# Performance work log

Hardware: AMD Instinct MI355X
Metric: run time of the kernel (lower is better)

Reference implementation:

```python
import jax, jax.numpy as jnp
import numpy as np

N_NODES = 20000
L_MAX = 6
R_IN = 256
R_HID = 512
R_OUT = 256
LEAKY_SLOPE = 0.01  # torch.nn.functional.leaky_relu default


def setup_inputs() -> dict:
    key = jax.random.key(0)
    k1, k2, k3, k4 = jax.random.split(key, 4)
    x = jax.random.normal(k1, (N_NODES, R_IN, L_MAX * 2), dtype=jnp.float32)
    # per-node rotation angles -> per-degree 2x2 rotation matrices (k*theta for degree k)
    theta = jax.random.uniform(k2, (N_NODES,), dtype=jnp.float32, minval=0.0, maxval=2.0 * np.pi)
    ang = theta[:, None] * jnp.arange(1, L_MAX + 1, dtype=jnp.float32)[None, :]  # (n, L)
    c, s = jnp.cos(ang), jnp.sin(ang)
    rot_theta = jnp.stack([jnp.stack([c, -s], axis=-1),
                           jnp.stack([s, c], axis=-1)], axis=-2)  # (n, L, 2, 2)
    # xavier_normal: std = sqrt(2 / (fan_in + fan_out))
    W1 = jax.random.normal(k3, (L_MAX, R_HID, R_IN), dtype=jnp.float32) * np.sqrt(2.0 / (R_IN + R_HID))
    W2 = jax.random.normal(k4, (L_MAX, R_OUT, R_HID), dtype=jnp.float32) * np.sqrt(2.0 / (R_HID + R_OUT))
    return {"x": x, "rot_theta": rot_theta, "W1": W1, "W2": W2}


def so2_linear(x, W, r_out):
    # x: (n, r_in, L_max*2); W: (L_max, r_out, r_in)
    n = x.shape[0]
    x4 = x.reshape(n, -1, L_MAX, 2)              # (n, r_in, L, 2)
    out = jnp.einsum('nilc,loi->nolc', x4, W)    # fused block-diagonal GEMM over degrees
    return out.reshape(n, r_out, L_MAX * 2)


def rot_activation(x, rot):
    # rotate each degree-l 2-vector into local frame, apply leaky_relu, rotate back
    n = x.shape[0]
    x4 = x.reshape(n, -1, L_MAX, 2)                      # (n, r, L, 2)
    a = jnp.einsum('njlm,nlmc->njlc', x4, rot)           # x @ R per (node, degree)
    a = jnp.where(a >= 0, a, LEAKY_SLOPE * a)            # pointwise leaky_relu
    out = jnp.einsum('njlc,nlmc->njlm', a, rot)          # (act) @ R^T  (inverse rotation)
    return out.reshape(x.shape)


def reference(x, rot_theta, W1, W2):
    h = so2_linear(x, W1, R_HID)
    h = rot_activation(h, rot_theta)
    return so2_linear(h, W2, R_OUT)
```

## Files before the change

### kernel.cpp

```cpp
#include <hip/hip_runtime.h>
#include <stdint.h>


#define LMAX 6
#define NN 20000
#define RIN 256
#define RHID 512
#define ROUT 256
#define MTILE 64
#define NMT 626
#define MPAD (NMT*MTILE)

#define A2_STRIDE 272
#define GE_STRIDE 528

typedef __attribute__((ext_vector_type(8))) short short8;
typedef __attribute__((ext_vector_type(4))) float f32x4;

__device__ __forceinline__ uint16_t f2bf(float f) {
  uint32_t x = __builtin_bit_cast(uint32_t, f);
  x += 0x7fffu + ((x >> 16) & 1u);
  return (uint16_t)(x >> 16);
}
__device__ __forceinline__ float bf2f(uint16_t u) {
  return __builtin_bit_cast(float, ((uint32_t)u) << 16);
}

__device__ __forceinline__ f32x4 mfma16(short8 a, short8 b, f32x4 c) {
  return __builtin_amdgcn_mfma_f32_16x16x32_bf16(a, b, c, 0, 0, 0);
}

__global__ void prep_weights(const float* __restrict__ W1, const float* __restrict__ W2,
                             uint16_t* __restrict__ w1f, uint16_t* __restrict__ w2f) {
  int idx = blockIdx.x * 256 + threadIdx.x;
  if (idx >= LMAX * RHID * RIN) return;
  {
    int l = idx / (RHID * RIN);
    int rem = idx - l * (RHID * RIN);
    int o = rem >> 8;
    int i = rem & 255;
    int lane = ((i >> 3) & 3) * 16 + (o & 15);
    size_t dst = (size_t)l * (RHID * RIN) +
                 ((((size_t)(o >> 4) * 8 + (i >> 5)) * 64 + lane) * 8 + (i & 7));
    w1f[dst] = f2bf(W1[idx]);
  }
  {
    int l = idx / (ROUT * RHID);
    int rem = idx - l * (ROUT * RHID);
    int o = rem >> 9;
    int j = rem & 511;
    int lane = ((j >> 3) & 3) * 16 + (o & 15);
    size_t dst = (size_t)l * (ROUT * RHID) +
                 ((((size_t)(o >> 4) * 16 + (j >> 5)) * 64 + lane) * 8 + (j & 7));
    w2f[dst] = f2bf(W2[idx]);
  }
}

__global__ void prep_x(const float* __restrict__ x, const float* __restrict__ rot,
                       uint16_t* __restrict__ xr) {
  int t = blockIdx.x * 256 + threadIdx.x;
  if (t >= NN * RIN) return;
  int n = t >> 8, i = t & 255;
  const float4* xp = (const float4*)(x + (size_t)t * 12);
  float4 v0 = xp[0], v1 = xp[1], v2 = xp[2];
  float xv[12] = {v0.x, v0.y, v0.z, v0.w, v1.x, v1.y, v1.z, v1.w, v2.x, v2.y, v2.z, v2.w};
  const float* rp = rot + (size_t)n * 24;
#pragma unroll
  for (int l = 0; l < LMAX; ++l) {
    float c0 = xv[2 * l], c1 = xv[2 * l + 1];
    float r00 = rp[4 * l + 0], r01 = rp[4 * l + 1];
    float r10 = rp[4 * l + 2], r11 = rp[4 * l + 3];
    float a0 = c0 * r00 + c1 * r10;
    float a1 = c0 * r01 + c1 * r11;
    size_t base = (size_t)l * MPAD * RIN + (size_t)(2 * n) * RIN + i;
    xr[base] = f2bf(a0);
    xr[base + RIN] = f2bf(a1);
  }
}

__global__ __launch_bounds__(512, 4) void so2_gemm(
    const uint16_t* __restrict__ xr,
    const uint16_t* __restrict__ w1f,
    const uint16_t* __restrict__ w2f,
    uint16_t* __restrict__ g) {
  __shared__ alignas(16) uint8_t SH[32768 + MTILE * A2_STRIDE];
  uint8_t* XsB = SH;
  uint8_t* A2B = SH + 32768;

  const int l = blockIdx.y;
  const int m0 = blockIdx.x * MTILE;
  const int tid = threadIdx.x;
  const int lane = tid & 63;
  const int wid = tid >> 6;
  const int l15 = lane & 15;
  const int l4 = lane >> 4;

  const char* xsrc = (const char*)(xr + (size_t)l * MPAD * RIN + (size_t)m0 * RIN);
#pragma unroll
  for (int it = 0; it < 4; ++it) {
    int off = it * 8192 + tid * 16;
    int row = off >> 9;
    int colb = off & 511;
    short8 v = *(const short8*)(xsrc + off);
    *(short8*)(XsB + row * 512 + (colb ^ ((row & 7) << 4))) = v;
  }
  __syncthreads();

  const uint16_t* w1p = w1f + (size_t)l * RHID * RIN;
  const uint16_t* w2p = w2f + (size_t)l * ROUT * RHID;

  f32x4 acc2[4][2];
#pragma unroll
  for (int a = 0; a < 4; ++a)
#pragma unroll
    for (int b = 0; b < 2; ++b)
      acc2[a][b] = (f32x4){0.f, 0.f, 0.f, 0.f};

#pragma unroll 1
  for (int oc = 0; oc < 4; ++oc) {
    f32x4 acc1[4];
#pragma unroll
    for (int a = 0; a < 4; ++a) acc1[a] = (f32x4){0.f, 0.f, 0.f, 0.f};

    const uint16_t* w1c = w1p + (((size_t)(oc * 8 + wid) * 8) * 64) * 8;
#pragma unroll
    for (int ks = 0; ks < 8; ++ks) {
      short8 bfr = *(const short8*)(w1c + ((size_t)ks * 64 + lane) * 8);
#pragma unroll
      for (int mf = 0; mf < 4; ++mf) {
        int row = mf * 16 + l15;
        int colb = ks * 64 + l4 * 16;
        short8 af = *(const short8*)(XsB + row * 512 + (colb ^ ((row & 7) << 4)));
        acc1[mf] = mfma16(af, bfr, acc1[mf]);
      }
    }

    __syncthreads();
#pragma unroll
    for (int mf = 0; mf < 4; ++mf)
#pragma unroll
      for (int r = 0; r < 4; ++r) {
        int row = mf * 16 + l4 * 4 + r;
        float v = acc1[mf][r];
        v = v >= 0.f ? v : 0.01f * v;
        *(uint16_t*)(A2B + row * A2_STRIDE + (wid * 16 + l15) * 2) = f2bf(v);
      }
    __syncthreads();

#pragma unroll
    for (int ks2 = 0; ks2 < 4; ++ks2) {
      short8 a2[4];
#pragma unroll
      for (int mf = 0; mf < 4; ++mf)
        a2[mf] = *(const short8*)(A2B + (mf * 16 + l15) * A2_STRIDE + ks2 * 64 + l4 * 16);
      short8 b2[2];
#pragma unroll
      for (int fc2 = 0; fc2 < 2; ++fc2) {
        int ofrag2 = wid * 2 + fc2;
        int kstep = oc * 4 + ks2;
        b2[fc2] = *(const short8*)(w2p + (((size_t)(ofrag2 * 16 + kstep)) * 64 + lane) * 8);
      }
#pragma unroll
      for (int mf = 0; mf < 4; ++mf)
#pragma unroll
        for (int fc2 = 0; fc2 < 2; ++fc2)
          acc2[mf][fc2] = mfma16(a2[mf], b2[fc2], acc2[mf][fc2]);
    }
  }

  __syncthreads();
#pragma unroll
  for (int mf = 0; mf < 4; ++mf)
#pragma unroll
    for (int fc2 = 0; fc2 < 2; ++fc2)
#pragma unroll
      for (int r = 0; r < 4; ++r) {
        int row = mf * 16 + l4 * 4 + r;
        int col = wid * 32 + fc2 * 16 + l15;
        *(uint16_t*)(SH + row * GE_STRIDE + col * 2) = f2bf(acc2[mf][fc2][r]);
      }
  __syncthreads();

  char* gdst = (char*)(g + (size_t)l * MPAD * ROUT + (size_t)m0 * ROUT);
#pragma unroll
  for (int it = 0; it < 4; ++it) {
    int off = it * 8192 + tid * 16;
    int row = off >> 9;
    int colb = off & 511;
    short8 v = *(const short8*)(SH + row * GE_STRIDE + colb);
    *(short8*)(gdst + off) = v;
  }
}

__global__ void post_out(const uint16_t* __restrict__ g, const float* __restrict__ rot,
                         float* __restrict__ out) {
  int n = blockIdx.x;
  int o = threadIdx.x;
  const float* rp = rot + (size_t)n * 24;
  float res[12];
#pragma unroll
  for (int l = 0; l < LMAX; ++l) {
    size_t base = (size_t)l * MPAD * ROUT + (size_t)(2 * n) * ROUT + o;
    float g0 = bf2f(g[base]);
    float g1 = bf2f(g[base + ROUT]);
    res[2 * l]     = rp[4 * l + 0] * g0 + rp[4 * l + 1] * g1;
    res[2 * l + 1] = rp[4 * l + 2] * g0 + rp[4 * l + 3] * g1;
  }
  float4* op = (float4*)(out + (size_t)(n * 256 + o) * 12);
  op[0] = make_float4(res[0], res[1], res[2], res[3]);
  op[1] = make_float4(res[4], res[5], res[6], res[7]);
  op[2] = make_float4(res[8], res[9], res[10], res[11]);
}

extern "C" void kernel_launch(void* const* d_in, const int* in_sizes, int n_in,
                              void* d_out, int out_size, void* d_ws, size_t ws_size,
                              hipStream_t stream) {
  (void)in_sizes; (void)n_in; (void)out_size;
  const float* x   = (const float*)d_in[0];
  const float* rot = (const float*)d_in[1];
  const float* W1  = (const float*)d_in[2];
  const float* W2  = (const float*)d_in[3];
  float* out = (float*)d_out;

  const size_t xr_elems = (size_t)LMAX * MPAD * RIN;
  const size_t w_elems  = (size_t)LMAX * RHID * RIN;
  if (ws_size < (size_t)LMAX * MPAD * ROUT * 2) return;

  uint16_t* xr  = (uint16_t*)d_out;
  uint16_t* w1f = xr + xr_elems;
  uint16_t* w2f = w1f + w_elems;
  uint16_t* g   = (uint16_t*)d_ws;

  prep_weights<<<3072, 256, 0, stream>>>(W1, W2, w1f, w2f);
  prep_x<<<20000, 256, 0, stream>>>(x, rot, xr);
  dim3 gg(NMT, LMAX);
  so2_gemm<<<gg, 512, 0, stream>>>(xr, w1f, w2f, g);
  post_out<<<20000, 256, 0, stream>>>(g, rot, out);
}
```

Baseline: 309.6 us.

## Persist GEMM blocks over multiple M tiles with double-buffered hidden activations

Each block of the fused two-GEMM kernel now handles four consecutive 64-row tiles instead of one. The hidden activation buffer is double-buffered so the second GEMM on one chunk overlaps the first GEMM on the next, which halves the barriers per chunk. Waves are rearranged into a 2x4 grid in place of 1x8, and the output is written straight from registers instead of being staged through shared memory. This trades fewer blocks (about 157x6) and more LDS per block for less barrier stalling and more register reuse, but the uncoalesced 2-byte global stores and lower parallelism could hurt.

After: 593.3 us. 91.6% more time.

```diff
diff --git a/kernel.cpp b/kernel.cpp
--- a/kernel.cpp
+++ b/kernel.cpp
@@ -10,9 +10,10 @@
 #define MTILE 64
 #define NMT 626
 #define MPAD (NMT*MTILE)
+#define TILES 4
+#define NBX ((NMT + TILES - 1) / TILES)
 
 #define A2_STRIDE 272
-#define GE_STRIDE 528
 
 typedef __attribute__((ext_vector_type(8))) short short8;
 typedef __attribute__((ext_vector_type(4))) float f32x4;
@@ -83,113 +84,143 @@
     const uint16_t* __restrict__ w1f,
     const uint16_t* __restrict__ w2f,
     uint16_t* __restrict__ g) {
-  __shared__ alignas(16) uint8_t SH[32768 + MTILE * A2_STRIDE];
-  uint8_t* XsB = SH;
-  uint8_t* A2B = SH + 32768;
+  __shared__ alignas(16) uint8_t Xs[MTILE * 512];
+  __shared__ alignas(16) uint8_t A2[2][MTILE * A2_STRIDE];
 
   const int l = blockIdx.y;
-  const int m0 = blockIdx.x * MTILE;
+  const int tile0 = blockIdx.x * TILES;
+  const int Tv = min(TILES, NMT - tile0);
   const int tid = threadIdx.x;
   const int lane = tid & 63;
   const int wid = tid >> 6;
+  const int wn = wid & 3;
+  const int wm = wid >> 2;
   const int l15 = lane & 15;
   const int l4 = lane >> 4;
 
-  const char* xsrc = (const char*)(xr + (size_t)l * MPAD * RIN + (size_t)m0 * RIN);
-#pragma unroll
-  for (int it = 0; it < 4; ++it) {
-    int off = it * 8192 + tid * 16;
-    int row = off >> 9;
-    int colb = off & 511;
-    short8 v = *(const short8*)(xsrc + off);
-    *(short8*)(XsB + row * 512 + (colb ^ ((row & 7) << 4))) = v;
-  }
+  const uint16_t* w1p = w1f + (size_t)l * (RHID * RIN);
+  const uint16_t* w2p = w2f + (size_t)l * (ROUT * RHID);
+  const uint16_t* xrl = xr + (size_t)l * MPAD * RIN;
+  uint16_t* gl = g + (size_t)l * MPAD * ROUT;
+
+  f32x4 acc1[2][2];
+  f32x4 acc2[2][4];
+#pragma unroll
+  for (int a = 0; a < 2; ++a)
+#pragma unroll
+    for (int b = 0; b < 4; ++b) acc2[a][b] = (f32x4){0.f, 0.f, 0.f, 0.f};
+
+  auto STAGE = [&](int t) {
+    const char* xsrc = (const char*)(xrl + (size_t)(tile0 + t) * MTILE * RIN);
+#pragma unroll
+    for (int it = 0; it < 4; ++it) {
+      int off = it * 8192 + tid * 16;
+      int row = off >> 9;
+      int colb = off & 511;
+      short8 v = *(const short8*)(xsrc + off);
+      *(short8*)(Xs + row * 512 + (colb ^ ((row & 7) << 4))) = v;
+    }
+  };
+
+  auto G1 = [&](int oc) {
+#pragma unroll
+    for (int a = 0; a < 2; ++a)
+#pragma unroll
+      for (int b = 0; b < 2; ++b) acc1[a][b] = (f32x4){0.f, 0.f, 0.f, 0.f};
+    const uint16_t* w1c0 = w1p + (size_t)(oc * 8 + wn * 2) * (8 * 64 * 8);
+    const uint16_t* w1c1 = w1c0 + 8 * 64 * 8;
+#pragma unroll
+    for (int ks = 0; ks < 8; ++ks) {
+      short8 b0 = *(const short8*)(w1c0 + ((size_t)ks * 64 + lane) * 8);
+      short8 b1 = *(const short8*)(w1c1 + ((size_t)ks * 64 + lane) * 8);
+#pragma unroll
+      for (int mf = 0; mf < 2; ++mf) {
+        int row = wm * 32 + mf * 16 + l15;
+        int colb = ks * 64 + l4 * 16;
+        short8 a = *(const short8*)(Xs + row * 512 + (colb ^ ((row & 7) << 4)));
+        acc1[mf][0] = mfma16(a, b0, acc1[mf][0]);
+        acc1[mf][1] = mfma16(a, b1, acc1[mf][1]);
+      }
+    }
+  };
+
+  auto WA2 = [&](int oc) {
+    uint8_t* buf = A2[oc & 1];
+#pragma unroll
+    for (int mf = 0; mf < 2; ++mf)
+#pragma unroll
+      for (int fc = 0; fc < 2; ++fc)
+#pragma unroll
+        for (int r = 0; r < 4; ++r) {
+          int row = wm * 32 + mf * 16 + l4 * 4 + r;
+          int col = wn * 32 + fc * 16 + l15;
+          float v = acc1[mf][fc][r];
+          v = v >= 0.f ? v : 0.01f * v;
+          *(uint16_t*)(buf + row * A2_STRIDE + col * 2) = f2bf(v);
+        }
+  };
+
+  auto G2 = [&](int oc) {
+    const uint8_t* buf = A2[oc & 1];
+#pragma unroll
+    for (int ks2 = 0; ks2 < 4; ++ks2) {
+      short8 a2[2];
+#pragma unroll
+      for (int mf = 0; mf < 2; ++mf)
+        a2[mf] = *(const short8*)(buf + (wm * 32 + mf * 16 + l15) * A2_STRIDE +
+                                  ks2 * 64 + l4 * 16);
+#pragma unroll
+      for (int nf = 0; nf < 4; ++nf) {
+        short8 b = *(const short8*)(w2p + ((size_t)((wn * 4 + nf) * 16 + oc * 4 + ks2) * 64 + lane) * 8);
+#pragma unroll
+        for (int mf = 0; mf < 2; ++mf)
+          acc2[mf][nf] = mfma16(a2[mf], b, acc2[mf][nf]);
+      }
+    }
+  };
+
+  auto EPI = [&](int t) {
+    uint16_t* gb = gl + (size_t)(tile0 + t) * MTILE * ROUT;
+#pragma unroll
+    for (int mf = 0; mf < 2; ++mf)
+#pragma unroll
+      for (int nf = 0; nf < 4; ++nf) {
+#pragma unroll
+        for (int r = 0; r < 4; ++r) {
+          int row = wm * 32 + mf * 16 + l4 * 4 + r;
+          int col = wn * 64 + nf * 16 + l15;
+          gb[(size_t)row * ROUT + col] = f2bf(acc2[mf][nf][r]);
+        }
+        acc2[mf][nf] = (f32x4){0.f, 0.f, 0.f, 0.f};
+      }
+  };
+
+  STAGE(0);
   __syncthreads();
-
-  const uint16_t* w1p = w1f + (size_t)l * RHID * RIN;
-  const uint16_t* w2p = w2f + (size_t)l * ROUT * RHID;
-
-  f32x4 acc2[4][2];
-#pragma unroll
-  for (int a = 0; a < 4; ++a)
-#pragma unroll
-    for (int b = 0; b < 2; ++b)
-      acc2[a][b] = (f32x4){0.f, 0.f, 0.f, 0.f};
-
-#pragma unroll 1
-  for (int oc = 0; oc < 4; ++oc) {
-    f32x4 acc1[4];
-#pragma unroll
-    for (int a = 0; a < 4; ++a) acc1[a] = (f32x4){0.f, 0.f, 0.f, 0.f};
-
-    const uint16_t* w1c = w1p + (((size_t)(oc * 8 + wid) * 8) * 64) * 8;
-#pragma unroll
-    for (int ks = 0; ks < 8; ++ks) {
-      short8 bfr = *(const short8*)(w1c + ((size_t)ks * 64 + lane) * 8);
-#pragma unroll
-      for (int mf = 0; mf < 4; ++mf) {
-        int row = mf * 16 + l15;
-        int colb = ks * 64 + l4 * 16;
-        short8 af = *(const short8*)(XsB + row * 512 + (colb ^ ((row & 7) << 4)));
-        acc1[mf] = mfma16(af, bfr, acc1[mf]);
-      }
-    }
-
-    __syncthreads();
-#pragma unroll
-    for (int mf = 0; mf < 4; ++mf)
-#pragma unroll
-      for (int r = 0; r < 4; ++r) {
-        int row = mf * 16 + l4 * 4 + r;
-        float v = acc1[mf][r];
-        v = v >= 0.f ? v : 0.01f * v;
-        *(uint16_t*)(A2B + row * A2_STRIDE + (wid * 16 + l15) * 2) = f2bf(v);
-      }
-    __syncthreads();
-
-#pragma unroll
-    for (int ks2 = 0; ks2 < 4; ++ks2) {
-      short8 a2[4];
-#pragma unroll
-      for (int mf = 0; mf < 4; ++mf)
-        a2[mf] = *(const short8*)(A2B + (mf * 16 + l15) * A2_STRIDE + ks2 * 64 + l4 * 16);
-      short8 b2[2];
-#pragma unroll
-      for (int fc2 = 0; fc2 < 2; ++fc2) {
-        int ofrag2 = wid * 2 + fc2;
-        int kstep = oc * 4 + ks2;
-        b2[fc2] = *(const short8*)(w2p + (((size_t)(ofrag2 * 16 + kstep)) * 64 + lane) * 8);
-      }
-#pragma unroll
-      for (int mf = 0; mf < 4; ++mf)
-#pragma unroll
-        for (int fc2 = 0; fc2 < 2; ++fc2)
-          acc2[mf][fc2] = mfma16(a2[mf], b2[fc2], acc2[mf][fc2]);
-    }
-  }
-
+  G1(0);
+  WA2(0);
   __syncthreads();
-#pragma unroll
-  for (int mf = 0; mf < 4; ++mf)
-#pragma unroll
-    for (int fc2 = 0; fc2 < 2; ++fc2)
-#pragma unroll
-      for (int r = 0; r < 4; ++r) {
-        int row = mf * 16 + l4 * 4 + r;
-        int col = wid * 32 + fc2 * 16 + l15;
-        *(uint16_t*)(SH + row * GE_STRIDE + col * 2) = f2bf(acc2[mf][fc2][r]);
-      }
-  __syncthreads();
-
-  char* gdst = (char*)(g + (size_t)l * MPAD * ROUT + (size_t)m0 * ROUT);
-#pragma unroll
-  for (int it = 0; it < 4; ++it) {
-    int off = it * 8192 + tid * 16;
-    int row = off >> 9;
-    int colb = off & 511;
-    short8 v = *(const short8*)(SH + row * GE_STRIDE + colb);
-    *(short8*)(gdst + off) = v;
-  }
+
+  for (int c = 1; c < 4 * Tv; ++c) {
+    int oc = c & 3;
+    if (oc == 0) {
+      int t = c >> 2;
+      G2(3);
+      STAGE(t);
+      EPI(t - 1);
+      __syncthreads();
+      G1(0);
+      WA2(0);
+      __syncthreads();
+    } else {
+      G2(oc - 1);
+      G1(oc);
+      WA2(oc);
+      __syncthreads();
+    }
+  }
+  G2(3);
+  EPI(Tv - 1);
 }
 
 __global__ void post_out(const uint16_t* __restrict__ g, const float* __restrict__ rot,
@@ -233,7 +264,7 @@
 
   prep_weights<<<3072, 256, 0, stream>>>(W1, W2, w1f, w2f);
   prep_x<<<20000, 256, 0, stream>>>(x, rot, xr);
-  dim3 gg(NMT, LMAX);
+  dim3 gg(NBX, LMAX);
   so2_gemm<<<gg, 512, 0, stream>>>(xr, w1f, w2f, g);
   post_out<<<20000, 256, 0, stream>>>(g, rot, out);
 }
```

## Switch fused SO2 GEMM to 32x32x16 MFMA with larger hidden chunks and XOR swizzle

Applied to the files above, without the earlier changes.

Replaces the 16x16x32 bf16 MFMA tiles with 32x32x16 tiles, repacking both weight matrices into the matching fragment layout. The hidden dimension is now processed in two chunks of 256 instead of four of 128, and the second GEMM splits waves 2x4 over rows and output columns. A full XOR swizzle replaces the padded LDS strides, and the output staging reuses the input buffer. The aim is fewer LDS fragment reads per FLOP and fewer barriers per tile. In exchange, the kernel holds larger accumulators per wave and uses 64KB of LDS, which may lower occupancy.

New measurement: 541.1 us. +74.7%, slower.

```diff
diff --git a/kernel.cpp b/kernel.cpp
--- a/kernel.cpp
+++ b/kernel.cpp
@@ -11,11 +11,8 @@
 #define NMT 626
 #define MPAD (NMT*MTILE)
 
-#define A2_STRIDE 272
-#define GE_STRIDE 528
-
 typedef __attribute__((ext_vector_type(8))) short short8;
-typedef __attribute__((ext_vector_type(4))) float f32x4;
+typedef __attribute__((ext_vector_type(16))) float f32x16;
 
 __device__ __forceinline__ uint16_t f2bf(float f) {
   uint32_t x = __builtin_bit_cast(uint32_t, f);
@@ -26,8 +23,12 @@
   return __builtin_bit_cast(float, ((uint32_t)u) << 16);
 }
 
-__device__ __forceinline__ f32x4 mfma16(short8 a, short8 b, f32x4 c) {
-  return __builtin_amdgcn_mfma_f32_16x16x32_bf16(a, b, c, 0, 0, 0);
+__device__ __forceinline__ f32x16 mfma32(short8 a, short8 b, f32x16 c) {
+  return __builtin_amdgcn_mfma_f32_32x32x16_bf16(a, b, c, 0, 0, 0);
+}
+
+__device__ __forceinline__ int swz512(int row, int colb) {
+  return row * 512 + ((((colb >> 4) ^ row) & 31) << 4) + (colb & 15);
 }
 
 __global__ void prep_weights(const float* __restrict__ W1, const float* __restrict__ W2,
@@ -39,9 +40,9 @@
     int rem = idx - l * (RHID * RIN);
     int o = rem >> 8;
     int i = rem & 255;
-    int lane = ((i >> 3) & 3) * 16 + (o & 15);
+    int lane = ((i >> 3) & 1) * 32 + (o & 31);
     size_t dst = (size_t)l * (RHID * RIN) +
-                 ((((size_t)(o >> 4) * 8 + (i >> 5)) * 64 + lane) * 8 + (i & 7));
+                 ((((size_t)(o >> 5) * 16 + (i >> 4)) * 64 + lane) * 8 + (i & 7));
     w1f[dst] = f2bf(W1[idx]);
   }
   {
@@ -49,9 +50,9 @@
     int rem = idx - l * (ROUT * RHID);
     int o = rem >> 9;
     int j = rem & 511;
-    int lane = ((j >> 3) & 3) * 16 + (o & 15);
+    int lane = ((j >> 3) & 1) * 32 + (o & 31);
     size_t dst = (size_t)l * (ROUT * RHID) +
-                 ((((size_t)(o >> 4) * 16 + (j >> 5)) * 64 + lane) * 8 + (j & 7));
+                 ((((size_t)(o >> 5) * 32 + (j >> 4)) * 64 + lane) * 8 + (j & 7));
     w2f[dst] = f2bf(W2[idx]);
   }
 }
@@ -83,17 +84,21 @@
     const uint16_t* __restrict__ w1f,
     const uint16_t* __restrict__ w2f,
     uint16_t* __restrict__ g) {
-  __shared__ alignas(16) uint8_t SH[32768 + MTILE * A2_STRIDE];
-  uint8_t* XsB = SH;
-  uint8_t* A2B = SH + 32768;
+  __shared__ alignas(16) uint8_t Xs[MTILE * 512];
+  __shared__ alignas(16) uint8_t A2[MTILE * 512];
 
   const int l = blockIdx.y;
   const int m0 = blockIdx.x * MTILE;
   const int tid = threadIdx.x;
   const int lane = tid & 63;
   const int wid = tid >> 6;
-  const int l15 = lane & 15;
-  const int l4 = lane >> 4;
+  const int l31 = lane & 31;
+  const int lh = lane >> 5;
+  const int wm = wid & 1;
+  const int wn4 = wid >> 1;
+
+  const uint16_t* w1p = w1f + (size_t)l * (RHID * RIN);
+  const uint16_t* w2p = w2f + (size_t)l * (ROUT * RHID);
 
   const char* xsrc = (const char*)(xr + (size_t)l * MPAD * RIN + (size_t)m0 * RIN);
 #pragma unroll
@@ -102,83 +107,76 @@
     int row = off >> 9;
     int colb = off & 511;
     short8 v = *(const short8*)(xsrc + off);
-    *(short8*)(XsB + row * 512 + (colb ^ ((row & 7) << 4))) = v;
-  }
-  __syncthreads();
-
-  const uint16_t* w1p = w1f + (size_t)l * RHID * RIN;
-  const uint16_t* w2p = w2f + (size_t)l * ROUT * RHID;
-
-  f32x4 acc2[4][2];
-#pragma unroll
-  for (int a = 0; a < 4; ++a)
-#pragma unroll
-    for (int b = 0; b < 2; ++b)
-      acc2[a][b] = (f32x4){0.f, 0.f, 0.f, 0.f};
-
-#pragma unroll 1
-  for (int oc = 0; oc < 4; ++oc) {
-    f32x4 acc1[4];
-#pragma unroll
-    for (int a = 0; a < 4; ++a) acc1[a] = (f32x4){0.f, 0.f, 0.f, 0.f};
-
-    const uint16_t* w1c = w1p + (((size_t)(oc * 8 + wid) * 8) * 64) * 8;
-#pragma unroll
-    for (int ks = 0; ks < 8; ++ks) {
-      short8 bfr = *(const short8*)(w1c + ((size_t)ks * 64 + lane) * 8);
-#pragma unroll
-      for (int mf = 0; mf < 4; ++mf) {
-        int row = mf * 16 + l15;
-        int colb = ks * 64 + l4 * 16;
-        short8 af = *(const short8*)(XsB + row * 512 + (colb ^ ((row & 7) << 4)));
-        acc1[mf] = mfma16(af, bfr, acc1[mf]);
+    *(short8*)(Xs + swz512(row, colb)) = v;
+  }
+  __syncthreads();
+
+  f32x16 acc1[2];
+  f32x16 acc2[2];
+#pragma unroll
+  for (int a = 0; a < 2; ++a) acc2[a] = (f32x16)(0.f);
+
+  auto G1 = [&](int oc) {
+#pragma unroll
+    for (int a = 0; a < 2; ++a) acc1[a] = (f32x16)(0.f);
+    const uint16_t* wc = w1p + (size_t)(oc * 8 + wid) * (16 * 64 * 8);
+#pragma unroll
+    for (int ks = 0; ks < 16; ++ks) {
+      short8 b = *(const short8*)(wc + ((size_t)ks * 64 + lane) * 8);
+#pragma unroll
+      for (int mf = 0; mf < 2; ++mf) {
+        int row = mf * 32 + l31;
+        short8 a = *(const short8*)(Xs + swz512(row, ks * 32 + lh * 16));
+        acc1[mf] = mfma32(a, b, acc1[mf]);
       }
     }
-
-    __syncthreads();
-#pragma unroll
-    for (int mf = 0; mf < 4; ++mf)
-#pragma unroll
-      for (int r = 0; r < 4; ++r) {
-        int row = mf * 16 + l4 * 4 + r;
+  };
+
+  auto WA2 = [&]() {
+#pragma unroll
+    for (int mf = 0; mf < 2; ++mf)
+#pragma unroll
+      for (int r = 0; r < 16; ++r) {
+        int row = mf * 32 + (r & 3) + 8 * (r >> 2) + 4 * lh;
+        int colb = (wid * 32 + l31) * 2;
         float v = acc1[mf][r];
         v = v >= 0.f ? v : 0.01f * v;
-        *(uint16_t*)(A2B + row * A2_STRIDE + (wid * 16 + l15) * 2) = f2bf(v);
+        *(uint16_t*)(A2 + swz512(row, colb)) = f2bf(v);
       }
-    __syncthreads();
-
-#pragma unroll
-    for (int ks2 = 0; ks2 < 4; ++ks2) {
-      short8 a2[4];
-#pragma unroll
-      for (int mf = 0; mf < 4; ++mf)
-        a2[mf] = *(const short8*)(A2B + (mf * 16 + l15) * A2_STRIDE + ks2 * 64 + l4 * 16);
-      short8 b2[2];
-#pragma unroll
-      for (int fc2 = 0; fc2 < 2; ++fc2) {
-        int ofrag2 = wid * 2 + fc2;
-        int kstep = oc * 4 + ks2;
-        b2[fc2] = *(const short8*)(w2p + (((size_t)(ofrag2 * 16 + kstep)) * 64 + lane) * 8);
+  };
+
+  auto G2 = [&](int oc) {
+#pragma unroll
+    for (int ks = 0; ks < 16; ++ks) {
+      int row = wm * 32 + l31;
+      short8 a = *(const short8*)(A2 + swz512(row, ks * 32 + lh * 16));
+#pragma unroll
+      for (int nf = 0; nf < 2; ++nf) {
+        short8 b = *(const short8*)(w2p +
+            ((size_t)((wn4 * 2 + nf) * 32 + oc * 16 + ks) * 64 + lane) * 8);
+        acc2[nf] = mfma32(a, b, acc2[nf]);
       }
-#pragma unroll
-      for (int mf = 0; mf < 4; ++mf)
-#pragma unroll
-        for (int fc2 = 0; fc2 < 2; ++fc2)
-          acc2[mf][fc2] = mfma16(a2[mf], b2[fc2], acc2[mf][fc2]);
     }
-  }
-
-  __syncthreads();
-#pragma unroll
-  for (int mf = 0; mf < 4; ++mf)
-#pragma unroll
-    for (int fc2 = 0; fc2 < 2; ++fc2)
-#pragma unroll
-      for (int r = 0; r < 4; ++r) {
-        int row = mf * 16 + l4 * 4 + r;
-        int col = wid * 32 + fc2 * 16 + l15;
-        *(uint16_t*)(SH + row * GE_STRIDE + col * 2) = f2bf(acc2[mf][fc2][r]);
-      }
+  };
+
+  G1(0);
+  WA2();
+  __syncthreads();
+  G2(0);
+  G1(1);
+  __syncthreads();
+  WA2();
+  __syncthreads();
+  G2(1);
+
+#pragma unroll
+  for (int nf = 0; nf < 2; ++nf)
+#pragma unroll
+    for (int r = 0; r < 16; ++r) {
+      int row = wm * 32 + (r & 3) + 8 * (r >> 2) + 4 * lh;
+      int colb = ((wn4 * 2 + nf) * 32 + l31) * 2;
+      *(uint16_t*)(Xs + swz512(row, colb)) = f2bf(acc2[nf][r]);
+    }
   __syncthreads();
 
   char* gdst = (char*)(g + (size_t)l * MPAD * ROUT + (size_t)m0 * ROUT);
@@ -187,7 +185,7 @@
     int off = it * 8192 + tid * 16;
     int row = off >> 9;
     int colb = off & 511;
-    short8 v = *(const short8*)(SH + row * GE_STRIDE + colb);
+    short8 v = *(const short8*)(Xs + swz512(row, colb));
     *(short8*)(gdst + off) = v;
   }
 }
```
